# Performance work log

Hardware: AMD Instinct MI355X
Metric: run time of the kernel (lower is better)

## Reference

```python
import jax, jax.numpy as jnp
import numpy as np

OUTDIM, INPUTDIM, DEGREE = 64, 512, 8


def setup_inputs() -> dict:
    key = jax.random.key(0)
    k1, k2 = jax.random.split(key)
    x = jax.random.normal(k1, (16, 4096, INPUTDIM), dtype=jnp.float32)
    # torch.randn(outdim, inputdim, degree) / (sqrt(inputdim)*sqrt(degree))
    coeffs = jax.random.normal(k2, (OUTDIM, INPUTDIM, DEGREE), dtype=jnp.float32)
    coeffs = coeffs / (np.sqrt(INPUTDIM) * np.sqrt(DEGREE))
    bias = jnp.zeros((1, OUTDIM), dtype=jnp.float32)
    return {"x": x, "coeffs": coeffs, "bias": bias}


def _legendre_basis(xn, degree):
    # Iterative (memoized) Legendre recurrence; xn in [-1, 1], shape [N, I].
    Ps = [jnp.ones_like(xn)]
    if degree > 1:
        Ps.append(xn)
    for n in range(2, degree):
        Ps.append(((2.0 * n - 1.0) * xn * Ps[-1] - (n - 1.0) * Ps[-2]) / n)
    return jnp.stack(Ps, axis=-1)  # [N, I, D]


def reference(x, coeffs, bias):
    outdim, inputdim, degree = coeffs.shape
    outshape = x.shape[:-1] + (outdim,)
    x2 = x.reshape(-1, inputdim)                      # [N, I]
    xmin, xmax = x2.min(), x2.max()                   # global min-max normalize
    xn = 2.0 * (x2 - xmin) / (xmax - xmin) - 1.0
    P = _legendre_basis(xn, degree)                   # [N, I, D]
    y = jnp.einsum("nid,oid->no", P, coeffs)          # contract input & degree
    y = y + bias                                      # [N, O]
    return y.reshape(outshape)
```

## Files before the change

### kernel.cpp

```cpp
#include <hip/hip_runtime.h>
#include <math.h>


typedef __bf16 bf16x8 __attribute__((ext_vector_type(8)));
typedef float f32x4 __attribute__((ext_vector_type(4)));

__device__ __forceinline__ void gload_lds16(const float* g, void* lds) {
  __builtin_amdgcn_global_load_lds(
      static_cast<const unsigned int*>(static_cast<const void*>(g)),
      static_cast<unsigned int*>(lds), 16, 0, 0);
}

__global__ __launch_bounds__(256) void k_pre(
    const float4* __restrict__ x4, int n4,
    float* __restrict__ pmn, float* __restrict__ pmx,
    const float* __restrict__ coeffs, bf16x8* __restrict__ Bws, int doprep)
{
  if (doprep && blockIdx.x < 128) {
    int t = blockIdx.x * 256 + threadIdx.x;
    int lane = t & 63;
    int tile = t >> 6;
    int ct = tile & 3;
    int kt = tile >> 2;
    int ii = kt * 4 + (lane >> 4);
    int o  = ct * 16 + (lane & 15);
    const float4* cp = (const float4*)(coeffs + ((size_t)o * 512 + ii) * 8);
    float4 c0 = cp[0], c1 = cp[1];
    bf16x8 v;
    v[0] = (__bf16)(c0.x);
    v[1] = (__bf16)(c0.y);
    v[2] = (__bf16)(c0.z * 1.5f);
    v[3] = (__bf16)(c0.w * 2.5f);
    v[4] = (__bf16)(c1.x * 4.375f);
    v[5] = (__bf16)(c1.y * 7.875f);
    v[6] = (__bf16)(c1.z * 14.4375f);
    v[7] = (__bf16)(c1.w * 26.8125f);
    Bws[(size_t)(kt * 4 + ct) * 64 + lane] = v;
  }
  float mn = 3.4e38f, mx = -3.4e38f;
  int stride = gridDim.x * 256;
  for (int i = blockIdx.x * 256 + threadIdx.x; i < n4; i += stride) {
    float4 v = x4[i];
    mn = fminf(mn, fminf(fminf(v.x, v.y), fminf(v.z, v.w)));
    mx = fmaxf(mx, fmaxf(fmaxf(v.x, v.y), fmaxf(v.z, v.w)));
  }
  #pragma unroll
  for (int off = 32; off > 0; off >>= 1) {
    mn = fminf(mn, __shfl_down(mn, off));
    mx = fmaxf(mx, __shfl_down(mx, off));
  }
  __shared__ float smn[4], smx[4];
  int w = threadIdx.x >> 6;
  if ((threadIdx.x & 63) == 0) { smn[w] = mn; smx[w] = mx; }
  __syncthreads();
  if (threadIdx.x == 0) {
    pmn[blockIdx.x] = fminf(fminf(smn[0], smn[1]), fminf(smn[2], smn[3]));
    pmx[blockIdx.x] = fmaxf(fmaxf(smx[0], smx[1]), fmaxf(smx[2], smx[3]));
  }
}

#define NPART 2048
__global__ __launch_bounds__(256, 2) void k_main(
    const float* __restrict__ x, const bf16x8* __restrict__ Bws,
    const float* __restrict__ bias, const float* __restrict__ pmn,
    const float* __restrict__ pmx, float* __restrict__ y)
{
  __shared__ __attribute__((aligned(16))) char smem[65536];

  const int t    = threadIdx.x;
  const int lane = t & 63;
  const int w    = t >> 6;
  const int m    = lane & 15;
  const int quad = lane >> 4;
  const size_t blockRow = (size_t)blockIdx.x * 128;

  const float* gp[8];
  #pragma unroll
  for (int p = 0; p < 8; ++p) {
    int r15 = (4 * p + quad) & 15;
    int row = 32 * w + 4 * p + quad;
    int cfl = m ^ r15;
    gp[p] = x + (size_t)(blockRow + row) * 512 + cfl * 4;
  }
  #pragma unroll
  for (int p = 0; p < 8; ++p)
    gload_lds16(gp[p], smem + (w * 8 + p) * 1024);

  float mn = 3.4e38f, mx = -3.4e38f;
  #pragma unroll
  for (int j = 0; j < NPART / 64; ++j) {
    mn = fminf(mn, pmn[lane + j * 64]);
    mx = fmaxf(mx, pmx[lane + j * 64]);
  }
  #pragma unroll
  for (int o2 = 32; o2 > 0; o2 >>= 1) {
    mn = fminf(mn, __shfl_xor(mn, o2));
    mx = fmaxf(mx, __shfl_xor(mx, o2));
  }
  const float s   = 2.0f / (mx - mn);
  const float off = fmaf(-mn, s, -1.0f);

  bf16x8 Bq[2][4];
  #pragma unroll
  for (int ct = 0; ct < 4; ++ct)
    Bq[0][ct] = Bws[(size_t)((4 * w + 0) * 4 + ct) * 64 + lane];

  f32x4 acc[8][4];
  #pragma unroll
  for (int f = 0; f < 8; ++f)
    #pragma unroll
    for (int ct = 0; ct < 4; ++ct) acc[f][ct] = (f32x4){0.f, 0.f, 0.f, 0.f};

  int xbase[8], xo[4];
  #pragma unroll
  for (int f = 0; f < 8; ++f) xbase[f] = (f * 16 + m) * 64 + quad;
  #pragma unroll
  for (int k = 0; k < 4; ++k) xo[k] = ((4 * w + k) ^ m) << 2;

  const float C2 = 0.33333334f, C3 = 0.26666668f, C4 = 0.25714287f;
  const float C5 = 0.25396827f, C6 = 0.25252524f, C7 = 0.25174826f;

  __syncthreads();

  for (int c = 0; c < 8; ++c) {
    const float* xr = (const float*)(smem + (c & 1) * 32768);

    if (c < 7) {
      char* lb = smem + ((c + 1) & 1) * 32768;
      #pragma unroll
      for (int p = 0; p < 8; ++p)
        gload_lds16(gp[p] + (c + 1) * 64, lb + (w * 8 + p) * 1024);
    }

    float xvv[2][8];
    #pragma unroll
    for (int f = 0; f < 8; ++f) xvv[0][f] = xr[xbase[f] + xo[0]];

    #pragma unroll
    for (int ktl = 0; ktl < 4; ++ktl) {
      const int l = c * 4 + ktl;

      {
        const int lp  = (l + 1) & 31;
        const int ktg = ((lp >> 2) << 4) + 4 * w + (lp & 3);
        #pragma unroll
        for (int ct = 0; ct < 4; ++ct)
          Bq[(ktl + 1) & 1][ct] = Bws[(size_t)(ktg * 4 + ct) * 64 + lane];
      }
      if (ktl < 3) {
        #pragma unroll
        for (int f = 0; f < 8; ++f)
          xvv[(ktl + 1) & 1][f] = xr[xbase[f] + xo[ktl + 1]];
      }

      #pragma unroll
      for (int f = 0; f < 8; ++f) {
        float xn = fmaf(xvv[ktl & 1][f], s, off);
        float s2 = fmaf(xn, xn, -C2);
        float s3 = (s2 - C3) * xn;
        float s4 = fmaf(xn, s3, -(C4 * s2));
        float s5 = fmaf(xn, s4, -(C5 * s3));
        float s6 = fmaf(xn, s5, -(C6 * s4));
        float s7 = fmaf(xn, s6, -(C7 * s5));
        bf16x8 av;
        av[0] = (__bf16)1.0f; av[1] = (__bf16)xn; av[2] = (__bf16)s2; av[3] = (__bf16)s3;
        av[4] = (__bf16)s4;   av[5] = (__bf16)s5; av[6] = (__bf16)s6; av[7] = (__bf16)s7;
        #pragma unroll
        for (int ct = 0; ct < 4; ++ct)
          acc[f][ct] = __builtin_amdgcn_mfma_f32_16x16x32_bf16(av, Bq[ktl & 1][ct], acc[f][ct], 0, 0, 0);
      }
    }
    __syncthreads();
  }

  f32x4* red = (f32x4*)smem;
  float bv0 = bias[m], bv1 = bias[16 + m], bv2 = bias[32 + m], bv3 = bias[48 + m];
  #pragma unroll
  for (int r = 0; r < 2; ++r) {
    if (r == 1) __syncthreads();
    #pragma unroll
    for (int g2 = 0; g2 < 4; ++g2) {
      if (g2 != w) {
        int slot = w - (w > g2 ? 1 : 0);
        #pragma unroll
        for (int ct = 0; ct < 4; ++ct)
          red[(size_t)g2 * 768 + slot * 256 + ct * 64 + lane] = acc[r * 4 + g2][ct];
      }
    }
    __syncthreads();
    #pragma unroll
    for (int g2 = 0; g2 < 4; ++g2) {
      if (g2 == w) {
        f32x4 vv[4];
        #pragma unroll
        for (int ct = 0; ct < 4; ++ct) {
          f32x4 v = acc[r * 4 + g2][ct];
          v += red[(size_t)g2 * 768 + 0 * 256 + ct * 64 + lane];
          v += red[(size_t)g2 * 768 + 1 * 256 + ct * 64 + lane];
          v += red[(size_t)g2 * 768 + 2 * 256 + ct * 64 + lane];
          vv[ct] = v;
        }
        float* yp = y + (blockRow + (r * 4 + g2) * 16 + quad * 4) * 64 + m;
        #pragma unroll
        for (int rr = 0; rr < 4; ++rr) {
          float* ypr = yp + rr * 64;
          ypr[0]  = vv[0][rr] + bv0;
          ypr[16] = vv[1][rr] + bv1;
          ypr[32] = vv[2][rr] + bv2;
          ypr[48] = vv[3][rr] + bv3;
        }
      }
    }
  }
}

__global__ __launch_bounds__(256) void k_so(
    const float* __restrict__ pmn, const float* __restrict__ pmx, int nb,
    float* __restrict__ so)
{
  float mn = 3.4e38f, mx = -3.4e38f;
  for (int i = threadIdx.x; i < nb; i += 256) {
    mn = fminf(mn, pmn[i]);
    mx = fmaxf(mx, pmx[i]);
  }
  #pragma unroll
  for (int off = 32; off > 0; off >>= 1) {
    mn = fminf(mn, __shfl_down(mn, off));
    mx = fmaxf(mx, __shfl_down(mx, off));
  }
  __shared__ float smn[4], smx[4];
  int w = threadIdx.x >> 6;
  if ((threadIdx.x & 63) == 0) { smn[w] = mn; smx[w] = mx; }
  __syncthreads();
  if (threadIdx.x == 0) {
    mn = fminf(fminf(smn[0], smn[1]), fminf(smn[2], smn[3]));
    mx = fmaxf(fmaxf(smx[0], smx[1]), fmaxf(smx[2], smx[3]));
    float r = mx - mn;
    so[0] = 2.0f / r;
    so[1] = -2.0f * mn / r - 1.0f;
  }
}

__global__ __launch_bounds__(256) void k_main_simple(
    const float* __restrict__ x, const float* __restrict__ coeffs,
    const float* __restrict__ bias, const float* __restrict__ so, float* __restrict__ y)
{
  const float s = so[0], off = so[1];
  const int lane = threadIdx.x & 63;
  const int w    = threadIdx.x >> 6;
  const int m    = lane & 15;
  const int quad = lane >> 4;
  const int rowA = blockIdx.x * 64 + w * 16 + m;
  const float* xp = x + (size_t)rowA * 512 + quad;

  f32x4 acc0 = {0.f,0.f,0.f,0.f}, acc1 = acc0, acc2 = acc0, acc3 = acc0;
  const float c3a = 5.f/3.f, c3b = 2.f/3.f, c6a = 11.f/6.f, c6b = 5.f/6.f, c7a = 13.f/7.f, c7b = 6.f/7.f;

  for (int kt = 0; kt < 128; ++kt) {
    float xv = xp[kt * 4];
    int i = kt * 4 + quad;
    bf16x8 b[4];
    #pragma unroll
    for (int ct = 0; ct < 4; ++ct) {
      const float* cp = coeffs + ((size_t)(ct * 16 + m) * 512 + i) * 8;
      #pragma unroll
      for (int j = 0; j < 8; ++j) b[ct][j] = (__bf16)cp[j];
    }
    float xn = fmaf(xv, s, off);
    float p2 = fmaf(1.5f * xn, xn, -0.5f);
    float p3 = fmaf(c3a * xn, p2, -(c3b * xn));
    float p4 = fmaf(1.75f * xn, p3, -(0.75f * p2));
    float p5 = fmaf(1.8f * xn, p4, -(0.8f * p3));
    float p6 = fmaf(c6a * xn, p5, -(c6b * p4));
    float p7 = fmaf(c7a * xn, p6, -(c7b * p5));
    bf16x8 a;
    a[0] = (__bf16)1.0f; a[1] = (__bf16)xn; a[2] = (__bf16)p2; a[3] = (__bf16)p3;
    a[4] = (__bf16)p4;   a[5] = (__bf16)p5; a[6] = (__bf16)p6; a[7] = (__bf16)p7;
    acc0 = __builtin_amdgcn_mfma_f32_16x16x32_bf16(a, b[0], acc0, 0, 0, 0);
    acc1 = __builtin_amdgcn_mfma_f32_16x16x32_bf16(a, b[1], acc1, 0, 0, 0);
    acc2 = __builtin_amdgcn_mfma_f32_16x16x32_bf16(a, b[2], acc2, 0, 0, 0);
    acc3 = __builtin_amdgcn_mfma_f32_16x16x32_bf16(a, b[3], acc3, 0, 0, 0);
  }
  float b0v = bias[m], b1v = bias[16+m], b2v = bias[32+m], b3v = bias[48+m];
  float* yp = y + ((size_t)(blockIdx.x * 64 + w * 16 + quad * 4)) * 64 + m;
  #pragma unroll
  for (int r = 0; r < 4; ++r) {
    yp[r*64+ 0] = acc0[r] + b0v;
    yp[r*64+16] = acc1[r] + b1v;
    yp[r*64+32] = acc2[r] + b2v;
    yp[r*64+48] = acc3[r] + b3v;
  }
}

extern "C" void kernel_launch(void* const* d_in, const int* in_sizes, int n_in,
                              void* d_out, int out_size, void* d_ws, size_t ws_size,
                              hipStream_t stream)
{
  const float* x      = (const float*)d_in[0];
  const float* coeffs = (const float*)d_in[1];
  const float* bias   = (const float*)d_in[2];
  float* y = (float*)d_out;

  long nx = (long)in_sizes[0];
  int  N  = (int)(nx / 512);
  int  n4 = (int)(nx / 4);

  float*  so  = (float*)d_ws;
  float*  pmn = (float*)d_ws + 16;
  float*  pmx = pmn + 4096;
  bf16x8* Bws = (bf16x8*)((char*)d_ws + 65536);

  bool pre = ws_size >= (size_t)(65536 + 4096 * 64 * 2 + 4096);
  k_pre<<<NPART, 256, 0, stream>>>((const float4*)x, n4, pmn, pmx, coeffs, Bws, pre ? 1 : 0);
  if (pre) {
    k_main<<<N / 128, 256, 0, stream>>>(x, Bws, bias, pmn, pmx, y);
  } else {
    k_so<<<1, 256, 0, stream>>>(pmn, pmx, NPART, so);
    k_main_simple<<<N / 64, 256, 0, stream>>>(x, coeffs, bias, so, y);
  }
}
```

Before: 238.7 us.

## Fuse min-max reduction and Legendre GEMM into one cooperative grid-synced kernel

Replaces the separate pre-pass kernel (global min/max plus coefficient repacking) and main kernel with a single cooperative launch of 512 blocks. Each block reduces min/max over its own 128 rows, starts the first LDS tile load, and then does a grid-wide sync before finishing the global reduction and running the MFMA GEMM. This is meant to remove one kernel launch and one of the two full passes over x, since a block's rows may still be in L2 when it reads them again. It depends on all 512 blocks being co-resident at 2 blocks per CU, and adds the cost of a grid barrier; if the cooperative launch fails it falls back to the two-kernel path.

```diff
diff --git a/kernel.cpp b/kernel.cpp
--- a/kernel.cpp
+++ b/kernel.cpp
@@ -1,5 +1,8 @@
 #include <hip/hip_runtime.h>
+#include <hip/hip_cooperative_groups.h>
 #include <math.h>
+
+namespace cg = cooperative_groups;
 
 
 typedef __bf16 bf16x8 __attribute__((ext_vector_type(8)));
@@ -11,32 +14,219 @@
       static_cast<unsigned int*>(lds), 16, 0, 0);
 }
 
+__device__ __forceinline__ void bprep_tile(const float* __restrict__ coeffs,
+                                           bf16x8* __restrict__ Bws, int t) {
+  int lane = t & 63;
+  int tile = t >> 6;
+  int ct = tile & 3;
+  int kt = tile >> 2;
+  int ii = kt * 4 + (lane >> 4);
+  int o  = ct * 16 + (lane & 15);
+  const float4* cp = (const float4*)(coeffs + ((size_t)o * 512 + ii) * 8);
+  float4 c0 = cp[0], c1 = cp[1];
+  bf16x8 v;
+  v[0] = (__bf16)(c0.x);
+  v[1] = (__bf16)(c0.y);
+  v[2] = (__bf16)(c0.z * 1.5f);
+  v[3] = (__bf16)(c0.w * 2.5f);
+  v[4] = (__bf16)(c1.x * 4.375f);
+  v[5] = (__bf16)(c1.y * 7.875f);
+  v[6] = (__bf16)(c1.z * 14.4375f);
+  v[7] = (__bf16)(c1.w * 26.8125f);
+  Bws[(size_t)(kt * 4 + ct) * 64 + lane] = v;
+}
+
+#define NBLK 512
+__global__ __launch_bounds__(256, 2) void k_fused(
+    const float* __restrict__ x, const float* __restrict__ coeffs,
+    const float* __restrict__ bias, float* __restrict__ pmn,
+    float* __restrict__ pmx, bf16x8* __restrict__ Bws, float* __restrict__ y)
+{
+  __shared__ __attribute__((aligned(16))) char smem[65536];
+
+  const int t    = threadIdx.x;
+  const int lane = t & 63;
+  const int w    = t >> 6;
+  const int m    = lane & 15;
+  const int quad = lane >> 4;
+  const size_t blockRow = (size_t)blockIdx.x * 128;
+
+  if (blockIdx.x < 128)
+    bprep_tile(coeffs, Bws, blockIdx.x * 256 + t);
+
+  {
+    const float4* xt = (const float4*)(x + blockRow * 512);
+    float mn = 3.4e38f, mx = -3.4e38f;
+    #pragma unroll 8
+    for (int i = t; i < 16384; i += 256) {
+      float4 v = xt[i];
+      mn = fminf(mn, fminf(fminf(v.x, v.y), fminf(v.z, v.w)));
+      mx = fmaxf(mx, fmaxf(fmaxf(v.x, v.y), fmaxf(v.z, v.w)));
+    }
+    #pragma unroll
+    for (int o2 = 32; o2 > 0; o2 >>= 1) {
+      mn = fminf(mn, __shfl_down(mn, o2));
+      mx = fmaxf(mx, __shfl_down(mx, o2));
+    }
+    float* sred = (float*)(smem + 32768);
+    if (lane == 0) { sred[w] = mn; sred[4 + w] = mx; }
+    __syncthreads();
+    if (t == 0) {
+      pmn[blockIdx.x] = fminf(fminf(sred[0], sred[1]), fminf(sred[2], sred[3]));
+      pmx[blockIdx.x] = fmaxf(fmaxf(sred[4], sred[5]), fmaxf(sred[6], sred[7]));
+    }
+  }
+
+  const float* gp[8];
+  #pragma unroll
+  for (int p = 0; p < 8; ++p) {
+    int r15 = (4 * p + quad) & 15;
+    int row = 32 * w + 4 * p + quad;
+    int cfl = m ^ r15;
+    gp[p] = x + (size_t)(blockRow + row) * 512 + cfl * 4;
+  }
+  #pragma unroll
+  for (int p = 0; p < 8; ++p)
+    gload_lds16(gp[p], smem + (w * 8 + p) * 1024);
+
+  cg::this_grid().sync();
+
+  float mn = 3.4e38f, mx = -3.4e38f;
+  #pragma unroll
+  for (int j = 0; j < NBLK / 64; ++j) {
+    mn = fminf(mn, pmn[lane + j * 64]);
+    mx = fmaxf(mx, pmx[lane + j * 64]);
+  }
+  #pragma unroll
+  for (int o2 = 32; o2 > 0; o2 >>= 1) {
+    mn = fminf(mn, __shfl_xor(mn, o2));
+    mx = fmaxf(mx, __shfl_xor(mx, o2));
+  }
+  const float s   = 2.0f / (mx - mn);
+  const float off = fmaf(-mn, s, -1.0f);
+
+  bf16x8 Bq[2][4];
+  #pragma unroll
+  for (int ct = 0; ct < 4; ++ct)
+    Bq[0][ct] = Bws[(size_t)((4 * w + 0) * 4 + ct) * 64 + lane];
+
+  f32x4 acc[8][4];
+  #pragma unroll
+  for (int f = 0; f < 8; ++f)
+    #pragma unroll
+    for (int ct = 0; ct < 4; ++ct) acc[f][ct] = (f32x4){0.f, 0.f, 0.f, 0.f};
+
+  int xbase[8], xo[4];
+  #pragma unroll
+  for (int f = 0; f < 8; ++f) xbase[f] = (f * 16 + m) * 64 + quad;
+  #pragma unroll
+  for (int k = 0; k < 4; ++k) xo[k] = ((4 * w + k) ^ m) << 2;
+
+  const float C2 = 0.33333334f, C3 = 0.26666668f, C4 = 0.25714287f;
+  const float C5 = 0.25396827f, C6 = 0.25252524f, C7 = 0.25174826f;
+
+  __syncthreads();
+
+  for (int c = 0; c < 8; ++c) {
+    const float* xr = (const float*)(smem + (c & 1) * 32768);
+
+    if (c < 7) {
+      char* lb = smem + ((c + 1) & 1) * 32768;
+      #pragma unroll
+      for (int p = 0; p < 8; ++p)
+        gload_lds16(gp[p] + (c + 1) * 64, lb + (w * 8 + p) * 1024);
+    }
+
+    float xvv[2][8];
+    #pragma unroll
+    for (int f = 0; f < 8; ++f) xvv[0][f] = xr[xbase[f] + xo[0]];
+
+    #pragma unroll
+    for (int ktl = 0; ktl < 4; ++ktl) {
+      const int l = c * 4 + ktl;
+
+      {
+        const int lp  = (l + 1) & 31;
+        const int ktg = ((lp >> 2) << 4) + 4 * w + (lp & 3);
+        #pragma unroll
+        for (int ct = 0; ct < 4; ++ct)
+          Bq[(ktl + 1) & 1][ct] = Bws[(size_t)(ktg * 4 + ct) * 64 + lane];
+      }
+      if (ktl < 3) {
+        #pragma unroll
+        for (int f = 0; f < 8; ++f)
+          xvv[(ktl + 1) & 1][f] = xr[xbase[f] + xo[ktl + 1]];
+      }
+
+      #pragma unroll
+      for (int f = 0; f < 8; ++f) {
+        float xn = fmaf(xvv[ktl & 1][f], s, off);
+        float s2 = fmaf(xn, xn, -C2);
+        float s3 = (s2 - C3) * xn;
+        float s4 = fmaf(xn, s3, -(C4 * s2));
+        float s5 = fmaf(xn, s4, -(C5 * s3));
+        float s6 = fmaf(xn, s5, -(C6 * s4));
+        float s7 = fmaf(xn, s6, -(C7 * s5));
+        bf16x8 av;
+        av[0] = (__bf16)1.0f; av[1] = (__bf16)xn; av[2] = (__bf16)s2; av[3] = (__bf16)s3;
+        av[4] = (__bf16)s4;   av[5] = (__bf16)s5; av[6] = (__bf16)s6; av[7] = (__bf16)s7;
+        #pragma unroll
+        for (int ct = 0; ct < 4; ++ct)
+          acc[f][ct] = __builtin_amdgcn_mfma_f32_16x16x32_bf16(av, Bq[ktl & 1][ct], acc[f][ct], 0, 0, 0);
+      }
+    }
+    __syncthreads();
+  }
+
+  f32x4* red = (f32x4*)smem;
+  float bv0 = bias[m], bv1 = bias[16 + m], bv2 = bias[32 + m], bv3 = bias[48 + m];
+  #pragma unroll
+  for (int r = 0; r < 2; ++r) {
+    if (r == 1) __syncthreads();
+    #pragma unroll
+    for (int g2 = 0; g2 < 4; ++g2) {
+      if (g2 != w) {
+        int slot = w - (w > g2 ? 1 : 0);
+        #pragma unroll
+        for (int ct = 0; ct < 4; ++ct)
+          red[(size_t)g2 * 768 + slot * 256 + ct * 64 + lane] = acc[r * 4 + g2][ct];
+      }
+    }
+    __syncthreads();
+    #pragma unroll
+    for (int g2 = 0; g2 < 4; ++g2) {
+      if (g2 == w) {
+        f32x4 vv[4];
+        #pragma unroll
+        for (int ct = 0; ct < 4; ++ct) {
+          f32x4 v = acc[r * 4 + g2][ct];
+          v += red[(size_t)g2 * 768 + 0 * 256 + ct * 64 + lane];
+          v += red[(size_t)g2 * 768 + 1 * 256 + ct * 64 + lane];
+          v += red[(size_t)g2 * 768 + 2 * 256 + ct * 64 + lane];
+          vv[ct] = v;
+        }
+        float* yp = y + (blockRow + (r * 4 + g2) * 16 + quad * 4) * 64 + m;
+        #pragma unroll
+        for (int rr = 0; rr < 4; ++rr) {
+          float* ypr = yp + rr * 64;
+          ypr[0]  = vv[0][rr] + bv0;
+          ypr[16] = vv[1][rr] + bv1;
+          ypr[32] = vv[2][rr] + bv2;
+          ypr[48] = vv[3][rr] + bv3;
+        }
+      }
+    }
+  }
+}
+
+#define NPART 2048
 __global__ __launch_bounds__(256) void k_pre(
     const float4* __restrict__ x4, int n4,
     float* __restrict__ pmn, float* __restrict__ pmx,
     const float* __restrict__ coeffs, bf16x8* __restrict__ Bws, int doprep)
 {
-  if (doprep && blockIdx.x < 128) {
-    int t = blockIdx.x * 256 + threadIdx.x;
-    int lane = t & 63;
-    int tile = t >> 6;
-    int ct = tile & 3;
-    int kt = tile >> 2;
-    int ii = kt * 4 + (lane >> 4);
-    int o  = ct * 16 + (lane & 15);
-    const float4* cp = (const float4*)(coeffs + ((size_t)o * 512 + ii) * 8);
-    float4 c0 = cp[0], c1 = cp[1];
-    bf16x8 v;
-    v[0] = (__bf16)(c0.x);
-    v[1] = (__bf16)(c0.y);
-    v[2] = (__bf16)(c0.z * 1.5f);
-    v[3] = (__bf16)(c0.w * 2.5f);
-    v[4] = (__bf16)(c1.x * 4.375f);
-    v[5] = (__bf16)(c1.y * 7.875f);
-    v[6] = (__bf16)(c1.z * 14.4375f);
-    v[7] = (__bf16)(c1.w * 26.8125f);
-    Bws[(size_t)(kt * 4 + ct) * 64 + lane] = v;
-  }
+  if (doprep && blockIdx.x < 128)
+    bprep_tile(coeffs, Bws, blockIdx.x * 256 + threadIdx.x);
   float mn = 3.4e38f, mx = -3.4e38f;
   int stride = gridDim.x * 256;
   for (int i = blockIdx.x * 256 + threadIdx.x; i < n4; i += stride) {
@@ -59,7 +249,6 @@
   }
 }
 
-#define NPART 2048
 __global__ __launch_bounds__(256, 2) void k_main(
     const float* __restrict__ x, const bf16x8* __restrict__ Bws,
     const float* __restrict__ bias, const float* __restrict__ pmn,
@@ -124,22 +313,18 @@
 
   for (int c = 0; c < 8; ++c) {
     const float* xr = (const float*)(smem + (c & 1) * 32768);
-
     if (c < 7) {
       char* lb = smem + ((c + 1) & 1) * 32768;
       #pragma unroll
       for (int p = 0; p < 8; ++p)
         gload_lds16(gp[p] + (c + 1) * 64, lb + (w * 8 + p) * 1024);
     }
-
     float xvv[2][8];
     #pragma unroll
     for (int f = 0; f < 8; ++f) xvv[0][f] = xr[xbase[f] + xo[0]];
-
     #pragma unroll
     for (int ktl = 0; ktl < 4; ++ktl) {
       const int l = c * 4 + ktl;
-
       {
         const int lp  = (l + 1) & 31;
         const int ktg = ((lp >> 2) << 4) + 4 * w + (lp & 3);
@@ -152,7 +337,6 @@
         for (int f = 0; f < 8; ++f)
           xvv[(ktl + 1) & 1][f] = xr[xbase[f] + xo[ktl + 1]];
       }
-
       #pragma unroll
       for (int f = 0; f < 8; ++f) {
         float xn = fmaf(xvv[ktl & 1][f], s, off);
@@ -311,6 +495,14 @@
   bf16x8* Bws = (bf16x8*)((char*)d_ws + 65536);
 
   bool pre = ws_size >= (size_t)(65536 + 4096 * 64 * 2 + 4096);
+  if (pre && N == 65536) {
+    void* args[] = {(void*)&x, (void*)&coeffs, (void*)&bias,
+                    (void*)&pmn, (void*)&pmx, (void*)&Bws, (void*)&y};
+    hipError_t e = hipLaunchCooperativeKernel((const void*)k_fused,
+                                              dim3(NBLK), dim3(256), args, 0, stream);
+    if (e == hipSuccess) return;
+    (void)hipGetLastError();
+  }
   k_pre<<<NPART, 256, 0, stream>>>((const float4*)x, n4, pmn, pmx, coeffs, Bws, pre ? 1 : 0);
   if (pre) {
     k_main<<<N / 128, 256, 0, stream>>>(x, Bws, bias, pmn, pmx, y);
```

After: 319.9 us. 1.34x slower.
